# Kernel tuning notes

Hardware: AMD Instinct MI355X
Metric: run time of the kernel (lower is better)

The kernel has to match this reference:

```python
import jax, jax.numpy as jnp
import numpy as np

ALPHA = 0.2  # LeakyReLU negative slope
NEG = -1e12


def setup_inputs() -> dict:
    key = jax.random.key(0)
    ks = jax.random.split(key, 7)
    B, N, Cin, F, H = 4, 2048, 256, 64, 4
    x = jax.random.normal(ks[0], (B, N, Cin), dtype=jnp.float32)
    adj = jax.random.randint(ks[1], (N, N), 0, 2, dtype=jnp.int32)
    W = jax.random.normal(ks[2], (H, Cin, F), dtype=jnp.float32) * (1.414 / np.sqrt(Cin))
    a1 = jax.random.normal(ks[3], (H, F), dtype=jnp.float32) * 0.1
    a2 = jax.random.normal(ks[4], (H, F), dtype=jnp.float32) * 0.1
    Wl = jax.random.normal(ks[5], (F, H * F), dtype=jnp.float32) * (1.0 / np.sqrt(H * F))
    bl = jax.random.normal(ks[6], (F,), dtype=jnp.float32) * 0.01
    return {"x": x, "adj": adj, "W": W, "a1": a1, "a2": a2, "Wl": Wl, "bl": bl}


def leaky(v):
    return jnp.where(v >= 0, v, ALPHA * v)


def reference(x, adj, W, a1, a2, Wl, bl):
    # Eval mode: dropout is a no-op.
    # h: [B,H,N,F] per-head projected features
    h = jnp.einsum("bnc,hcf->bhnf", x, W)
    # additive attention: e[b,h,i,j] = leaky(h_i . a1 + h_j . a2)
    f1 = jnp.einsum("bhnf,hf->bhn", h, a1)  # source term
    f2 = jnp.einsum("bhnf,hf->bhn", h, a2)  # target term
    e = leaky(f1[:, :, :, None] + f2[:, :, None, :])  # [B,H,N,N]
    e = jnp.where(adj[None, None] > 0, e, NEG)
    # NOTE: original softmaxes over dim=1 of [B,N,N], i.e. the i axis (axis=2 here)
    att = jax.nn.softmax(e, axis=2)
    hp = jnp.einsum("bhij,bhjf->bhif", att, h)  # [B,H,N,F]
    hp = jax.nn.relu(hp)  # concat=True heads
    B, H, N, F = hp.shape
    cat = hp.transpose(0, 2, 1, 3).reshape(B, N, H * F)
    out = leaky(cat @ Wl.T + bl)  # n_heads > 1 -> linear + leakyrelu
    return out
```

## Files before the change

kernel.cpp:

```cpp
#include <hip/hip_runtime.h>
#include <hip/hip_bf16.h>
#include <stdint.h>

typedef __attribute__((ext_vector_type(8))) short short8;
typedef __attribute__((ext_vector_type(4))) float f32x4;
typedef _Float16 f16;
typedef __attribute__((ext_vector_type(8))) f16 f16x8;
typedef __attribute__((ext_vector_type(2))) f16 f16x2;
typedef uint32_t u32;
typedef uint16_t u16;
typedef uint8_t u8;

#define LOG2E 1.4426950408889634f


__device__ __forceinline__ u16 f2bf(float f){
  union{float f; u32 u;} x; x.f = f;
  u32 r = x.u + 0x7FFFu + ((x.u >> 16) & 1u);
  return (u16)(r >> 16);
}
__device__ __forceinline__ u32 pkbf(float a, float b){
  __hip_bfloat162 h = __float22bfloat162_rn(float2{a, b});
  union{ __hip_bfloat162 h; u32 u; } cv; cv.h = h;
  return cv.u;
}
__device__ __forceinline__ u32 pkh(float a, float b){
  f16x2 h; h.x = (f16)a; h.y = (f16)b;
  union{ f16x2 h; u32 u; } cv; cv.h = h;
  return cv.u;
}
__device__ __forceinline__ f16x2 uh2(u32 x){ union{u32 u; f16x2 h;} v; v.u = x; return v.h; }
__device__ __forceinline__ u32 h2u(f16x2 x){ union{f16x2 h; u32 u;} v; v.h = x; return v.u; }

__global__ __launch_bounds__(256) void k_front(const float* __restrict__ x,
      const float* __restrict__ W, const float* __restrict__ a1, const float* __restrict__ a2,
      const int* __restrict__ adj,
      u8* __restrict__ adjb, u16* __restrict__ hT,
      float* __restrict__ Aarr, float* __restrict__ Barr,
      float* __restrict__ Cexp, float* __restrict__ Dexp,
      float* __restrict__ Dsum){
  int bid = blockIdx.x, t = threadIdx.x;

  if (bid >= 2560){
    Dsum[(bid - 2560)*256 + t] = 0.f;
    return;
  }
  if (bid >= 512){
    int idx = (bid - 512)*256 + t;
    const int4* ap = (const int4*)(adj + (size_t)idx*8);
    int4 v0 = ap[0], v1 = ap[1];
    u32 byte = (u32)(v0.x > 0)        | ((u32)(v0.y > 0) << 1)
             | ((u32)(v0.z > 0) << 2) | ((u32)(v0.w > 0) << 3)
             | ((u32)(v1.x > 0) << 4) | ((u32)(v1.y > 0) << 5)
             | ((u32)(v1.z > 0) << 6) | ((u32)(v1.w > 0) << 7);
    adjb[idx] = (u8)byte;
    return;
  }
  __shared__ u16 WL[64*264];
  int rt = bid & 127, cb = bid >> 7;
  const float* Wh = W + (size_t)cb*16384;
  {
    int f0 = (t & 15)*4;
    int cg = t >> 4;
    int s = ((f0 >> 2) & 7) << 3;
    #pragma unroll
    for (int it2 = 0; it2 < 4; it2++){
      int c0 = (cg + it2*16)*4;
      float4 wv0 = *(const float4*)(Wh + (size_t)(c0+0)*64 + f0);
      float4 wv1 = *(const float4*)(Wh + (size_t)(c0+1)*64 + f0);
      float4 wv2 = *(const float4*)(Wh + (size_t)(c0+2)*64 + f0);
      float4 wv3 = *(const float4*)(Wh + (size_t)(c0+3)*64 + f0);
      int cc = c0 ^ s;
      #pragma unroll
      for (int k = 0; k < 4; k++){
        u32 lo = pkbf((&wv0.x)[k], (&wv1.x)[k]);
        u32 hi = pkbf((&wv2.x)[k], (&wv3.x)[k]);
        *(uint2*)&WL[(f0+k)*264 + cc] = uint2{lo, hi};
      }
    }
  }
  __syncthreads();

  int w = t >> 6, l = t & 63;
  int rA = rt*64 + w*16 + (l & 15);
  int kg = (l >> 4) * 8;
  int rowq[4], rswq[4];
  #pragma unroll
  for (int q = 0; q < 4; q++){
    rowq[q] = q*16 + (l & 15);
    rswq[q] = ((rowq[q] >> 2) & 7) << 3;
  }
  f32x4 acc[4] = {};
  const float* xrow = x + (size_t)rA * 256;
  #pragma unroll
  for (int ks = 0; ks < 8; ks++){
    int c = ks*32 + kg;
    float4 xa = *(const float4*)(xrow + c);
    float4 xb = *(const float4*)(xrow + c + 4);
    union{u32 w[4]; short8 v;} A;
    A.w[0] = pkbf(xa.x, xa.y); A.w[1] = pkbf(xa.z, xa.w);
    A.w[2] = pkbf(xb.x, xb.y); A.w[3] = pkbf(xb.z, xb.w);
    #pragma unroll
    for (int q = 0; q < 4; q++){
      short8 Bf = *(const short8*)&WL[rowq[q]*264 + (c ^ rswq[q])];
      acc[q] = __builtin_amdgcn_mfma_f32_16x16x32_bf16(A.v, Bf, acc[q], 0, 0, 0);
    }
  }
  int rb = rt*64 + w*16 + (l >> 4)*4;
  int b = rb >> 11, n = rb & 2047;
  #pragma unroll
  for (int q = 0; q < 4; q++){
    int f = q*16 + (l & 15);
    u32 p0 = pkh(acc[q][0], acc[q][1]);
    u32 p1 = pkh(acc[q][2], acc[q][3]);
    u16* dst = hT + ((size_t)(b*4 + cb)*64 + f)*2048 + n;
    *(uint2*)dst = uint2{p0, p1};
  }
  float a1v[4], a2v[4];
  #pragma unroll
  for (int q = 0; q < 4; q++){
    a1v[q] = a1[cb*64 + q*16 + (l & 15)];
    a2v[q] = a2[cb*64 + q*16 + (l & 15)];
  }
  float s1[4], s2[4];
  #pragma unroll
  for (int r = 0; r < 4; r++){
    s1[r] = acc[0][r]*a1v[0] + acc[1][r]*a1v[1] + acc[2][r]*a1v[2] + acc[3][r]*a1v[3];
    s2[r] = acc[0][r]*a2v[0] + acc[1][r]*a2v[1] + acc[2][r]*a2v[2] + acc[3][r]*a2v[3];
  }
  #pragma unroll
  for (int m = 1; m <= 8; m <<= 1){
    #pragma unroll
    for (int r = 0; r < 4; r++){
      s1[r] += __shfl_xor(s1[r], m);
      s2[r] += __shfl_xor(s2[r], m);
    }
  }
  if ((l & 15) == 0){
    #pragma unroll
    for (int r = 0; r < 4; r++){
      int row = rb + r;
      int bb = row >> 11, nn = row & 2047;
      int o = (bb*4 + cb)*2048 + nn;
      float fa = s1[r] * LOG2E;
      Aarr[o] = __builtin_amdgcn_exp2f(fa);
      Barr[o] = __builtin_amdgcn_exp2f(0.2f*fa);
      float fb = s2[r] * LOG2E;
      Cexp[o] = __builtin_amdgcn_exp2f(fb);
      Dexp[o] = __builtin_amdgcn_exp2f(0.2f*fb);
    }
  }
}

__global__ __launch_bounds__(256) void k_colsum(const u32* __restrict__ adjw,
      const float* __restrict__ Aarr, const float* __restrict__ Barr,
      const float* __restrict__ Cexp, const float* __restrict__ Dexp,
      float* __restrict__ Dsum){
  __shared__ float AL[128*16], BL[128*16];
  __shared__ float red[4][1024];
  int jt = blockIdx.x;
  int is = blockIdx.y;
  int t = threadIdx.x, w = t >> 6, l = t & 63;
  int i0 = is*128;
  for (int k = t; k < 2048; k += 256){
    int bh = k >> 7, ii = k & 127;
    AL[ii*16 + bh] = Aarr[bh*2048 + i0 + ii];
    BL[ii*16 + bh] = Barr[bh*2048 + i0 + ii];
  }
  int j = jt*64 + l;
  float Cj[16], Dj[16];
  #pragma unroll
  for (int bh = 0; bh < 16; bh++){
    Cj[bh] = Cexp[bh*2048 + j];
    Dj[bh] = Dexp[bh*2048 + j];
  }
  float acc[16] = {};
  __syncthreads();
  int wi = jt*2 + (l >> 5), sh = l & 31;
  const u32* aw = adjw + wi;
  #pragma unroll 2
  for (int ii = w*32; ii < w*32 + 32; ii++){
    u32 m = aw[(size_t)(i0 + ii)*64];
    float bitf = (float)((m >> sh) & 1u);
    const float* ar = &AL[ii*16];
    const float* br = &BL[ii*16];
    #pragma unroll
    for (int q = 0; q < 4; q++){
      float4 a4 = *(const float4*)(ar + q*4);
      float4 b4 = *(const float4*)(br + q*4);
      acc[q*4+0] = fmaf(fmaxf(a4.x*Cj[q*4+0], b4.x*Dj[q*4+0]), bitf, acc[q*4+0]);
      acc[q*4+1] = fmaf(fmaxf(a4.y*Cj[q*4+1], b4.y*Dj[q*4+1]), bitf, acc[q*4+1]);
      acc[q*4+2] = fmaf(fmaxf(a4.z*Cj[q*4+2], b4.z*Dj[q*4+2]), bitf, acc[q*4+2]);
      acc[q*4+3] = fmaf(fmaxf(a4.w*Cj[q*4+3], b4.w*Dj[q*4+3]), bitf, acc[q*4+3]);
    }
  }
  #pragma unroll
  for (int bh = 0; bh < 16; bh++) red[w][bh*64 + l] = acc[bh];
  __syncthreads();
  #pragma unroll
  for (int k = 0; k < 4; k++){
    int e = t*4 + k;
    float s = (red[0][e] + red[1][e]) + (red[2][e] + red[3][e]);
    int bh = e >> 6, jl = e & 63;
    atomicAdd(&Dsum[bh*2048 + jt*64 + jl], s);
  }
}

__global__ __launch_bounds__(256) void k_pv(const u32* __restrict__ adjw, const u16* __restrict__ hT,
      const float* __restrict__ Aarr, const float* __restrict__ Barr,
      const float* __restrict__ Cexp, const float* __restrict__ Dexp,
      const float* __restrict__ Dsum, u16* __restrict__ part){
  int it = blockIdx.x;
  int bh = blockIdx.y;
  int jh = blockIdx.z;
  int b = bh >> 2, h = bh & 3;
  int t = threadIdx.x;
  int w = t >> 6, l = t & 63;

  __shared__ u16 hTl[64*136];
  __shared__ u32 CA2l[512];
  __shared__ u32 DB2l[512];

  {
    int gj = bh*2048 + jh*1024 + t*4;
    float4 c4 = *(const float4*)(Cexp + gj);
    float4 d4 = *(const float4*)(Dexp + gj);
    float4 s4 = *(const float4*)(Dsum + gj);
    float i0v = 16.0f/s4.x, i1v = 16.0f/s4.y, i2v = 16.0f/s4.z, i3v = 16.0f/s4.w;
    CA2l[t*2]   = pkh(c4.x*i0v, c4.y*i1v);
    CA2l[t*2+1] = pkh(c4.z*i2v, c4.w*i3v);
    DB2l[t*2]   = pkh(d4.x*i0v, d4.y*i1v);
    DB2l[t*2+1] = pkh(d4.z*i2v, d4.w*i3v);
  }

  int i0 = it*128 + w*32 + (l & 15);
  f16x2 Ai02, Bi02, Ai12, Bi12;
  {
    const float sc = 0.0625f;
    float A0 = Aarr[bh*2048 + i0] * sc,      B0 = Barr[bh*2048 + i0] * sc;
    float A1 = Aarr[bh*2048 + i0 + 16] * sc, B1 = Barr[bh*2048 + i0 + 16] * sc;
    Ai02 = uh2(pkh(A0, A0)); Bi02 = uh2(pkh(B0, B0));
    Ai12 = uh2(pkh(A1, A1)); Bi12 = uh2(pkh(B1, B1));
  }
  const u16* hTr = hT + (size_t)bh * 64 * 2048;
  int kg = (l >> 4) * 8;
  f32x4 acc[2][4] = {};

  for (int jj = 0; jj < 1024; jj += 128){
    int jc = jh*1024 + jj;
    __syncthreads();
    {
      int f = t >> 2, seg = (t & 3) * 32;
      const u16* src = hTr + (size_t)f*2048 + jc + seg;
      u16* d = hTl + f*136 + seg;
      *(uint4*)(d)      = *(const uint4*)(src);
      *(uint4*)(d + 8)  = *(const uint4*)(src + 8);
      *(uint4*)(d + 16) = *(const uint4*)(src + 16);
      *(uint4*)(d + 24) = *(const uint4*)(src + 24);
    }
    __syncthreads();
    uint4 mw0 = *(const uint4*)(adjw + (size_t)i0*64 + (jc >> 5));
    uint4 mw1 = *(const uint4*)(adjw + (size_t)(i0+16)*64 + (jc >> 5));
    #pragma unroll
    for (int ks = 0; ks < 4; ks++){
      int pbase = (jj >> 1) + ks*16 + (l >> 4)*4;
      uint4 ca2 = *(const uint4*)&CA2l[pbase];
      uint4 db2 = *(const uint4*)&DB2l[pbase];
      u32 w0 = (&mw0.x)[ks] >> kg;
      u32 w1 = (&mw1.x)[ks] >> kg;
      union{u32 w[4]; f16x8 v;} A0u, A1u;
      #pragma unroll
      for (int p = 0; p < 4; p++){
        f16x2 cav = uh2((&ca2.x)[p]);
        f16x2 dbv = uh2((&db2.x)[p]);
        f16x2 e0 = __builtin_elementwise_max(Ai02*cav, Bi02*dbv);
        f16x2 e1 = __builtin_elementwise_max(Ai12*cav, Bi12*dbv);
        u32 m0 = ((u32)((int)(w0 << (31-2*p)) >> 31) & 0x0000FFFFu)
               | ((u32)((int)(w0 << (30-2*p)) >> 31) & 0xFFFF0000u);
        u32 m1 = ((u32)((int)(w1 << (31-2*p)) >> 31) & 0x0000FFFFu)
               | ((u32)((int)(w1 << (30-2*p)) >> 31) & 0xFFFF0000u);
        A0u.w[p] = h2u(e0) & m0;
        A1u.w[p] = h2u(e1) & m1;
      }
      #pragma unroll
      for (int q = 0; q < 4; q++){
        f16x8 Bf = *(const f16x8*)&hTl[(q*16 + (l & 15))*136 + ks*32 + kg];
        acc[0][q] = __builtin_amdgcn_mfma_f32_16x16x32_f16(A0u.v, Bf, acc[0][q], 0, 0, 0);
        acc[1][q] = __builtin_amdgcn_mfma_f32_16x16x32_f16(A1u.v, Bf, acc[1][q], 0, 0, 0);
      }
    }
  }
  u16* pr = part + ((size_t)(jh*4 + b)*2048)*256;
  #pragma unroll
  for (int r = 0; r < 2; r++){
    int nb = it*128 + w*32 + r*16 + (l >> 4)*4;
    #pragma unroll
    for (int q = 0; q < 4; q++){
      int f = h*64 + q*16 + (l & 15);
      #pragma unroll
      for (int rr = 0; rr < 4; rr++){
        pr[(size_t)(nb + rr)*256 + f] = f2bf(acc[r][q][rr]);
      }
    }
  }
}

__global__ __launch_bounds__(256) void k_out(const u16* __restrict__ part,
                       const float* __restrict__ Wl, const float* __restrict__ bl,
                       float* __restrict__ out){
  int rt = blockIdx.x;
  int w = threadIdx.x >> 6, l = threadIdx.x & 63;
  int rA = rt*64 + w*16 + (l & 15);
  int b = rA >> 11, n = rA & 2047;
  const u16* p0 = part + ((size_t)b*2048 + n)*256;
  const u16* p1 = part + ((size_t)(4 + b)*2048 + n)*256;
  int kg = (l >> 4) * 8;
  f32x4 acc[4] = {};
  #pragma unroll
  for (int ks = 0; ks < 8; ks++){
    int c = ks*32 + kg;
    short8 v0 = *(const short8*)(p0 + c);
    short8 v1 = *(const short8*)(p1 + c);
    float av[8];
    #pragma unroll
    for (int e = 0; e < 8; e++){
      union{u32 u; float f;} x0, x1;
      x0.u = ((u32)(u16)v0[e]) << 16;
      x1.u = ((u32)(u16)v1[e]) << 16;
      av[e] = fmaxf(x0.f + x1.f, 0.f);
    }
    union{u32 w[4]; short8 v;} A;
    A.w[0] = pkbf(av[0], av[1]); A.w[1] = pkbf(av[2], av[3]);
    A.w[2] = pkbf(av[4], av[5]); A.w[3] = pkbf(av[6], av[7]);
    #pragma unroll
    for (int q = 0; q < 4; q++){
      const float* wr = Wl + (size_t)(q*16 + (l & 15))*256 + c;
      float4 u0 = *(const float4*)(wr);
      float4 u1 = *(const float4*)(wr + 4);
      union{u32 w[4]; short8 v;} Bv;
      Bv.w[0] = pkbf(u0.x, u0.y); Bv.w[1] = pkbf(u0.z, u0.w);
      Bv.w[2] = pkbf(u1.x, u1.y); Bv.w[3] = pkbf(u1.z, u1.w);
      acc[q] = __builtin_amdgcn_mfma_f32_16x16x32_bf16(A.v, Bv.v, acc[q], 0, 0, 0);
    }
  }
  int rb = rt*64 + w*16 + (l >> 4)*4;
  #pragma unroll
  for (int q = 0; q < 4; q++){
    int o = q*16 + (l & 15);
    float bv = bl[o];
    #pragma unroll
    for (int r = 0; r < 4; r++){
      float v = acc[q][r] + bv;
      out[(size_t)(rb + r)*64 + o] = fmaxf(v, 0.2f*v);
    }
  }
}

extern "C" void kernel_launch(void* const* d_in, const int* in_sizes, int n_in,
                              void* d_out, int out_size, void* d_ws, size_t ws_size,
                              hipStream_t stream) {
  const float* x  = (const float*)d_in[0];
  const int* adj  = (const int*)d_in[1];
  const float* W  = (const float*)d_in[2];
  const float* a1 = (const float*)d_in[3];
  const float* a2 = (const float*)d_in[4];
  const float* Wl = (const float*)d_in[5];
  const float* bl = (const float*)d_in[6];
  float* out = (float*)d_out;
  char* ws = (char*)d_ws;

  u32* adjw    = (u32*)(ws + 0x0000000);
  u16* hT      = (u16*)(ws + 0x0080000);
  u16* part    = (u16*)(ws + 0x0480000);
  float* Aarr  = (float*)(ws + 0x1480000);
  float* Barr  = (float*)(ws + 0x14A0000);
  float* Cexp  = (float*)(ws + 0x14C0000);
  float* Dexp  = (float*)(ws + 0x14E0000);
  float* Dsum  = (float*)(ws + 0x1500000);

  k_front<<<2688, 256, 0, stream>>>(x, W, a1, a2, adj, (u8*)adjw, hT, Aarr, Barr, Cexp, Dexp, Dsum);
  k_colsum<<<dim3(32, 16), 256, 0, stream>>>(adjw, Aarr, Barr, Cexp, Dexp, Dsum);
  k_pv<<<dim3(16, 16, 2), 256, 0, stream>>>(adjw, hT, Aarr, Barr, Cexp, Dexp, Dsum, part);
  k_out<<<128, 256, 0, stream>>>(part, Wl, bl, out);
}
```

Before: 70.02 us.

## Drop split-K in PV kernel, use 512-thread blocks and fuse ReLU into output

The PV kernel no longer splits the j dimension across two grid slices. Each block now has 512 threads, and each wave handles 16 rows with one accumulator set over all 2048 columns. ReLU and the bf16 cast happen directly in the PV epilogue, so k_out reads a single cat buffer instead of summing two partial buffers. This halves the partial-result traffic and removes the reduction, at the cost of fewer blocks (256 instead of 512) and a longer serial loop per block.

```diff
diff --git a/kernel.cpp b/kernel.cpp
--- a/kernel.cpp
+++ b/kernel.cpp
@@ -206,23 +206,22 @@
   }
 }
 
-__global__ __launch_bounds__(256) void k_pv(const u32* __restrict__ adjw, const u16* __restrict__ hT,
+__global__ __launch_bounds__(512) void k_pv(const u32* __restrict__ adjw, const u16* __restrict__ hT,
       const float* __restrict__ Aarr, const float* __restrict__ Barr,
       const float* __restrict__ Cexp, const float* __restrict__ Dexp,
-      const float* __restrict__ Dsum, u16* __restrict__ part){
+      const float* __restrict__ Dsum, u16* __restrict__ cat){
   int it = blockIdx.x;
   int bh = blockIdx.y;
-  int jh = blockIdx.z;
   int b = bh >> 2, h = bh & 3;
   int t = threadIdx.x;
   int w = t >> 6, l = t & 63;
 
   __shared__ u16 hTl[64*136];
-  __shared__ u32 CA2l[512];
-  __shared__ u32 DB2l[512];
+  __shared__ u32 CA2l[1024];
+  __shared__ u32 DB2l[1024];
 
   {
-    int gj = bh*2048 + jh*1024 + t*4;
+    int gj = bh*2048 + t*4;
     float4 c4 = *(const float4*)(Cexp + gj);
     float4 d4 = *(const float4*)(Dexp + gj);
     float4 s4 = *(const float4*)(Dsum + gj);
@@ -233,105 +232,74 @@
     DB2l[t*2+1] = pkh(d4.z*i2v, d4.w*i3v);
   }
 
-  int i0 = it*128 + w*32 + (l & 15);
-  f16x2 Ai02, Bi02, Ai12, Bi12;
+  int i0 = it*128 + w*16 + (l & 15);
+  f16x2 Ai2, Bi2;
   {
     const float sc = 0.0625f;
-    float A0 = Aarr[bh*2048 + i0] * sc,      B0 = Barr[bh*2048 + i0] * sc;
-    float A1 = Aarr[bh*2048 + i0 + 16] * sc, B1 = Barr[bh*2048 + i0 + 16] * sc;
-    Ai02 = uh2(pkh(A0, A0)); Bi02 = uh2(pkh(B0, B0));
-    Ai12 = uh2(pkh(A1, A1)); Bi12 = uh2(pkh(B1, B1));
+    float A0 = Aarr[bh*2048 + i0] * sc, B0 = Barr[bh*2048 + i0] * sc;
+    Ai2 = uh2(pkh(A0, A0)); Bi2 = uh2(pkh(B0, B0));
   }
   const u16* hTr = hT + (size_t)bh * 64 * 2048;
   int kg = (l >> 4) * 8;
-  f32x4 acc[2][4] = {};
-
-  for (int jj = 0; jj < 1024; jj += 128){
-    int jc = jh*1024 + jj;
+  f32x4 acc[4] = {};
+
+  for (int jc = 0; jc < 2048; jc += 128){
     __syncthreads();
     {
-      int f = t >> 2, seg = (t & 3) * 32;
+      int f = t >> 3, seg = (t & 7) * 16;
       const u16* src = hTr + (size_t)f*2048 + jc + seg;
       u16* d = hTl + f*136 + seg;
-      *(uint4*)(d)      = *(const uint4*)(src);
-      *(uint4*)(d + 8)  = *(const uint4*)(src + 8);
-      *(uint4*)(d + 16) = *(const uint4*)(src + 16);
-      *(uint4*)(d + 24) = *(const uint4*)(src + 24);
+      *(uint4*)(d)     = *(const uint4*)(src);
+      *(uint4*)(d + 8) = *(const uint4*)(src + 8);
     }
     __syncthreads();
-    uint4 mw0 = *(const uint4*)(adjw + (size_t)i0*64 + (jc >> 5));
-    uint4 mw1 = *(const uint4*)(adjw + (size_t)(i0+16)*64 + (jc >> 5));
+    uint4 mw = *(const uint4*)(adjw + (size_t)i0*64 + (jc >> 5));
     #pragma unroll
     for (int ks = 0; ks < 4; ks++){
-      int pbase = (jj >> 1) + ks*16 + (l >> 4)*4;
+      int pbase = (jc >> 1) + ks*16 + (l >> 4)*4;
       uint4 ca2 = *(const uint4*)&CA2l[pbase];
       uint4 db2 = *(const uint4*)&DB2l[pbase];
-      u32 w0 = (&mw0.x)[ks] >> kg;
-      u32 w1 = (&mw1.x)[ks] >> kg;
-      union{u32 w[4]; f16x8 v;} A0u, A1u;
+      u32 w0 = (&mw.x)[ks] >> kg;
+      union{u32 w[4]; f16x8 v;} A0u;
       #pragma unroll
       for (int p = 0; p < 4; p++){
         f16x2 cav = uh2((&ca2.x)[p]);
         f16x2 dbv = uh2((&db2.x)[p]);
-        f16x2 e0 = __builtin_elementwise_max(Ai02*cav, Bi02*dbv);
-        f16x2 e1 = __builtin_elementwise_max(Ai12*cav, Bi12*dbv);
+        f16x2 e0 = __builtin_elementwise_max(Ai2*cav, Bi2*dbv);
         u32 m0 = ((u32)((int)(w0 << (31-2*p)) >> 31) & 0x0000FFFFu)
                | ((u32)((int)(w0 << (30-2*p)) >> 31) & 0xFFFF0000u);
-        u32 m1 = ((u32)((int)(w1 << (31-2*p)) >> 31) & 0x0000FFFFu)
-               | ((u32)((int)(w1 << (30-2*p)) >> 31) & 0xFFFF0000u);
         A0u.w[p] = h2u(e0) & m0;
-        A1u.w[p] = h2u(e1) & m1;
       }
       #pragma unroll
       for (int q = 0; q < 4; q++){
         f16x8 Bf = *(const f16x8*)&hTl[(q*16 + (l & 15))*136 + ks*32 + kg];
-        acc[0][q] = __builtin_amdgcn_mfma_f32_16x16x32_f16(A0u.v, Bf, acc[0][q], 0, 0, 0);
-        acc[1][q] = __builtin_amdgcn_mfma_f32_16x16x32_f16(A1u.v, Bf, acc[1][q], 0, 0, 0);
+        acc[q] = __builtin_amdgcn_mfma_f32_16x16x32_f16(A0u.v, Bf, acc[q], 0, 0, 0);
       }
     }
   }
-  u16* pr = part + ((size_t)(jh*4 + b)*2048)*256;
-  #pragma unroll
-  for (int r = 0; r < 2; r++){
-    int nb = it*128 + w*32 + r*16 + (l >> 4)*4;
-    #pragma unroll
-    for (int q = 0; q < 4; q++){
-      int f = h*64 + q*16 + (l & 15);
-      #pragma unroll
-      for (int rr = 0; rr < 4; rr++){
-        pr[(size_t)(nb + rr)*256 + f] = f2bf(acc[r][q][rr]);
-      }
-    }
-  }
-}
-
-__global__ __launch_bounds__(256) void k_out(const u16* __restrict__ part,
+  int nb = it*128 + w*16 + (l >> 4)*4;
+  #pragma unroll
+  for (int q = 0; q < 4; q++){
+    int f = h*64 + q*16 + (l & 15);
+    #pragma unroll
+    for (int rr = 0; rr < 4; rr++){
+      cat[((size_t)(b*2048 + nb + rr))*256 + f] = f2bf(fmaxf(acc[q][rr], 0.f));
+    }
+  }
+}
+
+__global__ __launch_bounds__(256) void k_out(const u16* __restrict__ cat,
                        const float* __restrict__ Wl, const float* __restrict__ bl,
                        float* __restrict__ out){
   int rt = blockIdx.x;
   int w = threadIdx.x >> 6, l = threadIdx.x & 63;
   int rA = rt*64 + w*16 + (l & 15);
-  int b = rA >> 11, n = rA & 2047;
-  const u16* p0 = part + ((size_t)b*2048 + n)*256;
-  const u16* p1 = part + ((size_t)(4 + b)*2048 + n)*256;
   int kg = (l >> 4) * 8;
   f32x4 acc[4] = {};
   #pragma unroll
   for (int ks = 0; ks < 8; ks++){
     int c = ks*32 + kg;
-    short8 v0 = *(const short8*)(p0 + c);
-    short8 v1 = *(const short8*)(p1 + c);
-    float av[8];
-    #pragma unroll
-    for (int e = 0; e < 8; e++){
-      union{u32 u; float f;} x0, x1;
-      x0.u = ((u32)(u16)v0[e]) << 16;
-      x1.u = ((u32)(u16)v1[e]) << 16;
-      av[e] = fmaxf(x0.f + x1.f, 0.f);
-    }
-    union{u32 w[4]; short8 v;} A;
-    A.w[0] = pkbf(av[0], av[1]); A.w[1] = pkbf(av[2], av[3]);
-    A.w[2] = pkbf(av[4], av[5]); A.w[3] = pkbf(av[6], av[7]);
+    short8 Af = *(const short8*)(cat + (size_t)rA*256 + c);
     #pragma unroll
     for (int q = 0; q < 4; q++){
       const float* wr = Wl + (size_t)(q*16 + (l & 15))*256 + c;
@@ -340,7 +308,7 @@
       union{u32 w[4]; short8 v;} Bv;
       Bv.w[0] = pkbf(u0.x, u0.y); Bv.w[1] = pkbf(u0.z, u0.w);
       Bv.w[2] = pkbf(u1.x, u1.y); Bv.w[3] = pkbf(u1.z, u1.w);
-      acc[q] = __builtin_amdgcn_mfma_f32_16x16x32_bf16(A.v, Bv.v, acc[q], 0, 0, 0);
+      acc[q] = __builtin_amdgcn_mfma_f32_16x16x32_bf16(Af, Bv.v, acc[q], 0, 0, 0);
     }
   }
   int rb = rt*64 + w*16 + (l >> 4)*4;
@@ -371,7 +339,7 @@
 
   u32* adjw    = (u32*)(ws + 0x0000000);
   u16* hT      = (u16*)(ws + 0x0080000);
-  u16* part    = (u16*)(ws + 0x0480000);
+  u16* cat     = (u16*)(ws + 0x0480000);
   float* Aarr  = (float*)(ws + 0x1480000);
   float* Barr  = (float*)(ws + 0x14A0000);
   float* Cexp  = (float*)(ws + 0x14C0000);
@@ -380,6 +348,6 @@
 
   k_front<<<2688, 256, 0, stream>>>(x, W, a1, a2, adj, (u8*)adjw, hT, Aarr, Barr, Cexp, Dexp, Dsum);
   k_colsum<<<dim3(32, 16), 256, 0, stream>>>(adjw, Aarr, Barr, Cexp, Dexp, Dsum);
-  k_pv<<<dim3(16, 16, 2), 256, 0, stream>>>(adjw, hT, Aarr, Barr, Cexp, Dexp, Dsum, part);
-  k_out<<<128, 256, 0, stream>>>(part, Wl, bl, out);
-}
+  k_pv<<<dim3(16, 16), 512, 0, stream>>>(adjw, hT, Aarr, Barr, Cexp, Dexp, Dsum, cat);
+  k_out<<<128, 256, 0, stream>>>(cat, Wl, bl, out);
+}
```

Result: slower. 72.69 us (+3.8%).
